# Performance work log

Measured on AMD Instinct MI355X. Metric: run time of the kernel, lower is better.

The kernel has to match this reference:

```python
import jax, jax.numpy as jnp
import numpy as np

VOCAB, TAGS, EDIM, HDIM = 50000, 9, 256, 512
H = HDIM // 2  # per-direction LSTM hidden
B, S = 64, 512


def setup_inputs() -> dict:
    key = jax.random.key(0)
    ks = jax.random.split(key, 16)
    sc = 0.05
    inp = {
        'sentence_batch': jax.random.randint(ks[0], (B, S), 0, VOCAB),
        'tags_batch': jax.random.randint(ks[1], (B, S), 0, TAGS),
        'mask': jnp.ones((B, S), dtype=bool),
        'emb': jax.random.normal(ks[2], (VOCAB, EDIM), jnp.float32) * sc,
        'w_ih_f': jax.random.normal(ks[3], (4 * H, EDIM), jnp.float32) * sc,
        'w_hh_f': jax.random.normal(ks[4], (4 * H, H), jnp.float32) * sc,
        'b_ih_f': jnp.zeros((4 * H,), jnp.float32),
        'b_hh_f': jnp.zeros((4 * H,), jnp.float32),
        'w_ih_b': jax.random.normal(ks[5], (4 * H, EDIM), jnp.float32) * sc,
        'w_hh_b': jax.random.normal(ks[6], (4 * H, H), jnp.float32) * sc,
        'b_ih_b': jnp.zeros((4 * H,), jnp.float32),
        'b_hh_b': jnp.zeros((4 * H,), jnp.float32),
        'w_out': jax.random.normal(ks[7], (TAGS, HDIM), jnp.float32) * sc,
        'b_out': jnp.zeros((TAGS,), jnp.float32),
        'start_trans': jax.random.uniform(ks[8], (TAGS,), jnp.float32, -0.1, 0.1),
        'end_trans': jax.random.uniform(ks[9], (TAGS,), jnp.float32, -0.1, 0.1),
        'trans': jax.random.uniform(ks[10], (TAGS, TAGS), jnp.float32, -0.1, 0.1),
    }
    return inp


def _lstm_dir(x, w_ih, w_hh, b_ih, b_hh):
    # x: [B,S,E] -> [B,S,H], torch gate order (i,f,g,o)
    b, h = x.shape[0], w_hh.shape[1]
    xg = jnp.einsum('bse,ge->bsg', x, w_ih) + b_ih + b_hh  # precompute input gates

    def step(carry, xg_t):
        hprev, cprev = carry
        g = xg_t + hprev @ w_hh.T
        i, f, gg, o = jnp.split(g, 4, axis=-1)
        c = jax.nn.sigmoid(f) * cprev + jax.nn.sigmoid(i) * jnp.tanh(gg)
        hnew = jax.nn.sigmoid(o) * jnp.tanh(c)
        return (hnew, c), hnew

    init = (jnp.zeros((b, h), x.dtype), jnp.zeros((b, h), x.dtype))
    _, hs = jax.lax.scan(step, init, jnp.swapaxes(xg, 0, 1))
    return jnp.swapaxes(hs, 0, 1)


def _crf_nll(emissions, tags, mask, start_trans, end_trans, trans):
    # emissions [B,S,T], tags [B,S], mask [B,S] bool. torchcrf llh, reduction='mean'.
    b, s, t = emissions.shape
    mf = mask.astype(emissions.dtype)
    # numerator score
    em_sc = jnp.take_along_axis(emissions, tags[..., None], axis=-1)[..., 0]  # [B,S]
    tr_sc = trans[tags[:, :-1], tags[:, 1:]]  # [B,S-1]
    score = start_trans[tags[:, 0]] + em_sc[:, 0]
    score = score + jnp.sum((tr_sc + em_sc[:, 1:]) * mf[:, 1:], axis=-1)
    seq_ends = jnp.sum(mask.astype(jnp.int32), axis=1) - 1
    last_tags = jnp.take_along_axis(tags, seq_ends[:, None], axis=1)[:, 0]
    score = score + end_trans[last_tags]
    # partition via forward algorithm (scan over time)
    alpha0 = start_trans[None, :] + emissions[:, 0]  # [B,T]

    def step(alpha, inputs):
        em_t, m_t = inputs  # [B,T], [B]
        nxt = jax.nn.logsumexp(alpha[:, :, None] + trans[None] + em_t[:, None, :], axis=1)
        alpha = jnp.where(m_t[:, None], nxt, alpha)
        return alpha, None

    em_tm = jnp.swapaxes(emissions[:, 1:], 0, 1)  # [S-1,B,T]
    m_tm = jnp.swapaxes(mask[:, 1:], 0, 1)  # [S-1,B]
    alpha, _ = jax.lax.scan(step, alpha0, (em_tm, m_tm))
    logZ = jax.nn.logsumexp(alpha + end_trans[None, :], axis=-1)
    llh = score - logZ
    return -jnp.mean(llh)


def reference(sentence_batch, tags_batch, mask, emb,
              w_ih_f, w_hh_f, b_ih_f, b_hh_f,
              w_ih_b, w_hh_b, b_ih_b, b_hh_b,
              w_out, b_out, start_trans, end_trans, trans):
    x = emb[sentence_batch]  # [B,S,E]
    hf = _lstm_dir(x, w_ih_f, w_hh_f, b_ih_f, b_hh_f)
    hb = _lstm_dir(x[:, ::-1], w_ih_b, w_hh_b, b_ih_b, b_hh_b)[:, ::-1]
    feats = jnp.concatenate([hf, hb], axis=-1) @ w_out.T + b_out  # [B,S,TAGS]
    return _crf_nll(feats, tags_batch, mask, start_trans, end_trans, trans)
```

## Files before the change

kernel.cpp:

```cpp
#include <hip/hip_runtime.h>
#include <stdint.h>

typedef unsigned short u16;
typedef __attribute__((ext_vector_type(4))) float f32x4;
typedef __attribute__((ext_vector_type(8))) short short8;
typedef __attribute__((ext_vector_type(8))) int v8i;

#define OFF_BIAS   ((size_t)0)
#define OFF_WFRAG  ((size_t)8192)
#define OFF_HHIST  ((size_t)1048576)
#define OFF_FEATS  ((size_t)34603008)
#define OFF_XG     ((size_t)37748736)

__device__ __forceinline__ u16 f2bf(float f) {
  union { float f; uint32_t u; } v; v.f = f;
  uint32_t u = v.u;
  return (u16)((u + 0x7fffu + ((u >> 16) & 1u)) >> 16);
}
__device__ __forceinline__ float bf2f(u16 h) {
  union { uint32_t u; float f; } v; v.u = ((uint32_t)h) << 16; return v.f;
}
__device__ __forceinline__ float bfh(uint32_t wrd, int hh) {
  return bf2f((u16)(wrd >> (16 * hh)));
}
__device__ __forceinline__ short8 pack8(f32x4 a, f32x4 b) {
  short8 r;
  r[0] = (short)f2bf(a[0]); r[1] = (short)f2bf(a[1]);
  r[2] = (short)f2bf(a[2]); r[3] = (short)f2bf(a[3]);
  r[4] = (short)f2bf(b[0]); r[5] = (short)f2bf(b[1]);
  r[6] = (short)f2bf(b[2]); r[7] = (short)f2bf(b[3]);
  return r;
}

__global__ void bias_kernel(const float* __restrict__ bihf, const float* __restrict__ bhhf,
                            const float* __restrict__ bihb, const float* __restrict__ bhhb,
                            float* __restrict__ bias) {
  int n = blockIdx.x * 256 + threadIdx.x;
  if (n < 1024) bias[n] = bihf[n] + bhhf[n];
  else          bias[n] = bihb[n - 1024] + bhhb[n - 1024];
}

__global__ void wfrag_prep_kernel(const float* __restrict__ whhf,
                                  const float* __restrict__ whhb,
                                  uint8_t* __restrict__ wfrag) {
  int gid = blockIdx.x * 256 + threadIdx.x;
  const int l    = gid & 63;
  const int kt   = (gid >> 6) & 7;
  const int gate = (gid >> 9) & 3;
  const int ubi  = (gid >> 11) & 1;
  const int w    = (gid >> 12) & 7;
  const int d    = (gid >> 15) & 1;
  const float* W = d ? whhb : whhf;
  const int n = l & 15, q = l >> 4;
  const int row = gate * 256 + w * 32 + ubi * 16 + n;
  uint32_t out[2] = {0u, 0u};
  #pragma unroll
  for (int jj = 0; jj < 4; ++jj) {
    const int k0 = kt * 32 + q * 8 + jj * 2;
    const int k1 = k0 + 1;
    const int u0 = (k0 >> 5) * 32 + (k0 & 1) * 16 + ((k0 & 31) >> 1);
    const int u1 = (k1 >> 5) * 32 + (k1 & 1) * 16 + ((k1 & 31) >> 1);
    const float f0 = W[(size_t)row * 256 + u0] * 16.0f;
    const float f1 = W[(size_t)row * 256 + u1] * 16.0f;
    const int pk = __builtin_amdgcn_cvt_pk_fp8_f32(f0, f1, 0, false);
    out[jj >> 1] |= (uint32_t)(pk & 0xffff) << (16 * (jj & 1));
  }
  const int p = kt >> 2, cc = kt & 3;
  const size_t addr =
      ((((size_t)((d * 8 + w) * 2 + ubi) * 4 + gate) * 2 + p) * 64 + l) * 32 + (size_t)cc * 8;
  *(uint2*)(wfrag + addr) = make_uint2(out[0], out[1]);
}

__global__ void __launch_bounds__(256) xg_gemm_kernel(
    const int* __restrict__ sent, const float* __restrict__ emb,
    const float* __restrict__ w_ih_f, const float* __restrict__ w_ih_b,
    const float* __restrict__ bias, u16* __restrict__ xgf)
{
  extern __shared__ char smem[];
  u16*   Al    = (u16*)smem;
  u16*   Bl    = (u16*)(smem + 34816);
  float* biasl = (float*)(smem + 69632);
  int*   tokl  = (int*)(smem + 70144);

  const int tid = threadIdx.x;
  const int d  = blockIdx.x >> 3, u0 = (blockIdx.x & 7) * 32;
  const int g  = blockIdx.y >> 6, qb = (blockIdx.y >> 4) & 3, s0 = (blockIdx.y & 15) * 32;
  const float* wih = d ? w_ih_b : w_ih_f;

  if (tid < 128) {
    tokl[tid]  = sent[(size_t)(g * 16 + qb * 4 + (tid & 3)) * 512 + s0 + (tid >> 2)];
    biasl[tid] = bias[d * 1024 + (tid >> 5) * 256 + u0 + (tid & 31)];
  }
  __syncthreads();

  f32x4 acc[4][4];
  #pragma unroll
  for (int i = 0; i < 4; ++i)
    #pragma unroll
    for (int j = 0; j < 4; ++j) acc[i][j] = (f32x4){0.f, 0.f, 0.f, 0.f};

  const int wv = tid >> 6, l = tid & 63;
  const int mh = (wv >> 1) * 64, nh = (wv & 1) * 64;
  const int fr = l & 15, fq = l >> 4;
  const int rr = tid >> 1, c0 = (tid & 1) * 64;

  for (int kc = 0; kc < 2; ++kc) {
    const int k0 = kc * 128;
    const float* asrc = emb + (size_t)tokl[rr] * 256 + k0 + c0;
    const float* bsrc = wih + (size_t)((rr >> 5) * 256 + u0 + (rr & 31)) * 256 + k0 + c0;
    u16* adst = Al + rr * 136 + c0;
    u16* bdst = Bl + rr * 136 + c0;
    #pragma unroll
    for (int gdx = 0; gdx < 8; ++gdx) {
      f32x4 a0 = *(const f32x4*)(asrc + gdx * 8);
      f32x4 a1 = *(const f32x4*)(asrc + gdx * 8 + 4);
      *(short8*)(adst + gdx * 8) = pack8(a0, a1);
      f32x4 b0 = *(const f32x4*)(bsrc + gdx * 8);
      f32x4 b1 = *(const f32x4*)(bsrc + gdx * 8 + 4);
      *(short8*)(bdst + gdx * 8) = pack8(b0, b1);
    }
    __syncthreads();
    #pragma unroll
    for (int ks = 0; ks < 4; ++ks) {
      short8 af[4], bfr[4];
      #pragma unroll
      for (int i = 0; i < 4; ++i)
        af[i] = *(const short8*)(Al + (mh + i * 16 + fr) * 136 + ks * 32 + fq * 8);
      #pragma unroll
      for (int j = 0; j < 4; ++j)
        bfr[j] = *(const short8*)(Bl + (nh + j * 16 + fr) * 136 + ks * 32 + fq * 8);
      #pragma unroll
      for (int i = 0; i < 4; ++i)
        #pragma unroll
        for (int j = 0; j < 4; ++j)
          acc[i][j] = __builtin_amdgcn_mfma_f32_16x16x32_bf16(af[i], bfr[j], acc[i][j], 0, 0, 0);
    }
    __syncthreads();
  }

  const float LOG2E = 1.4426950408889634f;
  const int g0 = nh >> 5;
  const float sA = (g0 == 2) ? (2.0f * LOG2E) : (-LOG2E);
  const int mh4 = mh >> 2;
  const int tid2 = (u0 >> 5) * 64 + qb * 16 + fr;
  u16* xbase = xgf + ((size_t)(d * 4 + g) * 512) * 16384;
  #pragma unroll
  for (int i = 0; i < 4; ++i) {
    const int s = s0 + mh4 + i * 4 + fq;
    #pragma unroll
    for (int nsub = 0; nsub < 2; ++nsub) {
      const int j0 = nsub, j1 = nsub + 2;
      const int cA = nh + j0 * 16 + fr, cB = nh + j1 * 16 + fr;
      short8 sv;
      #pragma unroll
      for (int r = 0; r < 4; ++r) {
        float vA = (acc[i][j0][r] + biasl[cA]) * sA;
        float vB = (acc[i][j1][r] + biasl[cB]) * (-LOG2E);
        sv[r]     = (short)f2bf(vA);
        sv[4 + r] = (short)f2bf(vB);
      }
      *(short8*)(xbase + (size_t)s * 16384 + tid2 * 32 + nsub * 16 + g0 * 4) = sv;
    }
  }
}

template<int CB, int PW>
__device__ __forceinline__ void lstm_step(
    int T, int d, int l, int q, int n, int w, int tid,
    const v8i (&wv)[2][4][2], float (&cst)[2][4],
    uint4& X0, uint4& X1, uint4& X2, uint4& X3,
    uint8_t* hx, const u16* xsl, u16* hhb)
{
  const int t_eff = d ? (511 - T) : T;

  int tn = T + 2; if (tn > 511) tn = 511;
  const int sn = d ? (511 - tn) : tn;
  const uint4* pf = (const uint4*)(xsl + (size_t)sn * 16384);
  const uint4 P0 = pf[0], P1 = pf[1], P2 = pf[2], P3 = pf[3];

  const uint8_t* hr = hx + CB * 4224 + (l & 15) * 264 + q * 8;
  const int2 b0 = *(const int2*)(hr +   0);
  const int2 b1 = *(const int2*)(hr +  32);
  const int2 b2 = *(const int2*)(hr +  64);
  const int2 b3 = *(const int2*)(hr +  96);
  const int2 b4 = *(const int2*)(hr + 128);
  const int2 b5 = *(const int2*)(hr + 160);
  const int2 b6 = *(const int2*)(hr + 192);
  const int2 b7 = *(const int2*)(hr + 224);
  const v8i A0 = (v8i){b0.x, b0.y, b1.x, b1.y, b2.x, b2.y, b3.x, b3.y};
  const v8i A1 = (v8i){b4.x, b4.y, b5.x, b5.y, b6.x, b6.y, b7.x, b7.y};

  f32x4 acc[2][4];
  #pragma unroll
  for (int ubi = 0; ubi < 2; ++ubi)
    #pragma unroll
    for (int gate = 0; gate < 4; ++gate) {
      f32x4 a = (f32x4){0.f, 0.f, 0.f, 0.f};
      a = __builtin_amdgcn_mfma_scale_f32_16x16x128_f8f6f4(
              A0, wv[ubi][gate][0], a, 0, 0, 0, 0x7f7f7f7f, 0, 0x7f7f7f7f);
      a = __builtin_amdgcn_mfma_scale_f32_16x16x128_f8f6f4(
              A1, wv[ubi][gate][1], a, 0, 0, 0, 0x7f7f7f7f, 0, 0x7f7f7f7f);
      acc[ubi][gate] = a;
    }

  const float Sm = -0.0056355275f;
  const float Sg =  0.0112710550f;
  const float K2 =  2.8853900818f;
  float hval[2][4];
  #pragma unroll
  for (int ubi = 0; ubi < 2; ++ubi) {
    const uint4& Xa = ubi ? X2 : X0;
    const uint4& Xb = ubi ? X3 : X1;
    #pragma unroll
    for (int r = 0; r < 4; ++r) {
      const uint32_t wi = (r < 2) ? Xa.x : Xa.y;
      const uint32_t wf = (r < 2) ? Xa.z : Xa.w;
      const uint32_t wg = (r < 2) ? Xb.x : Xb.y;
      const uint32_t wo = (r < 2) ? Xb.z : Xb.w;
      const int hp = r & 1;
      const float argi = fmaf(acc[ubi][0][r], Sm, bfh(wi, hp));
      const float argf = fmaf(acc[ubi][1][r], Sm, bfh(wf, hp));
      const float argg = fmaf(acc[ubi][2][r], Sg, bfh(wg, hp));
      const float argo = fmaf(acc[ubi][3][r], Sm, bfh(wo, hp));
      const float Ei = __builtin_amdgcn_exp2f(argi);
      const float Ef = __builtin_amdgcn_exp2f(argf);
      const float Eg = __builtin_amdgcn_exp2f(argg);
      const float Eo = __builtin_amdgcn_exp2f(argo);
      const float pf_ = 1.0f + Ef, pi_ = 1.0f + Ei, pg_ = 1.0f + Eg;
      const float P  = pi_ * pg_;
      const float rD = __builtin_amdgcn_rcpf(P * pf_);
      const float num = fmaf(cst[ubi][r], P, fmaf(Eg, pf_, -pf_));
      const float c   = num * rD;
      cst[ubi][r] = c;
      const float E2 = __builtin_amdgcn_exp2f(c * K2);
      const float rQ = __builtin_amdgcn_rcpf((1.0f + E2) * (1.0f + Eo));
      hval[ubi][r] = fmaf(E2, rQ, -rQ);
    }
  }

  {
    uint8_t* hw = hx + PW * 4224 + w * 32 + 2 * n;
    #pragma unroll
    for (int r = 0; r < 4; ++r) {
      const int pk = __builtin_amdgcn_cvt_pk_fp8_f32(hval[0][r] * 16.0f,
                                                     hval[1][r] * 16.0f, 0, false);
      *(u16*)(hw + (q * 4 + r) * 264) = (u16)(pk & 0xffff);
    }
  }

  asm volatile("s_waitcnt lgkmcnt(0)" ::: "memory");
  __builtin_amdgcn_s_barrier();
  __builtin_amdgcn_sched_barrier(0);

  {
    u16* hhs = hhb + (size_t)t_eff * 256;
    #pragma unroll
    for (int r = 0; r < 4; ++r) {
      uint32_t pb;
      asm("v_cvt_pk_bf16_f32 %0, %1, %2" : "=v"(pb) : "v"(hval[0][r]), "v"(hval[1][r]));
      hhs[(size_t)(q * 4 + r) * 512 * 256]      = (u16)(pb & 0xffffu);
      hhs[(size_t)(q * 4 + r) * 512 * 256 + 16] = (u16)(pb >> 16);
    }
  }

  X0 = P0; X1 = P1; X2 = P2; X3 = P3;
}

__global__ void __launch_bounds__(512, 2) lstm_kernel(
    const u16* __restrict__ xgf, const uint8_t* __restrict__ wfrag,
    u16* __restrict__ hhist)
{
  __shared__ uint8_t hx[2 * 16 * 264];

  const int tid = threadIdx.x;
  const int bid = blockIdx.x;
  const int d = bid >> 2, g = bid & 3;
  const int w = tid >> 6, l = tid & 63;
  const int n = l & 15, q = l >> 4;

  v8i wv[2][4][2];
  {
    const uint8_t* wb = wfrag + (size_t)(d * 8 + w) * 32768;
    #pragma unroll
    for (int ubi = 0; ubi < 2; ++ubi)
      #pragma unroll
      for (int gate = 0; gate < 4; ++gate)
        #pragma unroll
        for (int p = 0; p < 2; ++p) {
          const uint8_t* src = wb + ((size_t)(((ubi * 4 + gate) * 2 + p) * 64 + l)) * 32;
          const uint4 lo = *(const uint4*)(src);
          const uint4 hi = *(const uint4*)(src + 16);
          wv[ubi][gate][p] = (v8i){(int)lo.x, (int)lo.y, (int)lo.z, (int)lo.w,
                                   (int)hi.x, (int)hi.y, (int)hi.z, (int)hi.w};
        }
  }

  for (int i = tid; i < 2112; i += 512) ((uint32_t*)hx)[i] = 0u;

  const u16* xsl = xgf + (size_t)(d * 4 + g) * 512 * 16384 + (size_t)tid * 32;
  float cst[2][4] = {};
  u16* hhb = hhist + ((size_t)(d * 64 + g * 16) * 512) * 256 + (w * 32 + n);

  uint4 X0, X1, X2, X3, Y0, Y1, Y2, Y3;
  {
    const uint4* p0 = (const uint4*)(xsl + (size_t)(d ? 511 : 0) * 16384);
    X0 = p0[0]; X1 = p0[1]; X2 = p0[2]; X3 = p0[3];
    const uint4* p1 = (const uint4*)(xsl + (size_t)(d ? 510 : 1) * 16384);
    Y0 = p1[0]; Y1 = p1[1]; Y2 = p1[2]; Y3 = p1[3];
  }
  __syncthreads();

  for (int tt = 0; tt < 512; tt += 2) {
    lstm_step<0, 1>(tt,     d, l, q, n, w, tid, wv, cst, X0, X1, X2, X3, hx, xsl, hhb);
    lstm_step<1, 0>(tt + 1, d, l, q, n, w, tid, wv, cst, Y0, Y1, Y2, Y3, hx, xsl, hhb);
  }
}

__global__ void __launch_bounds__(256) proj_kernel(
    const u16* __restrict__ hhist, const float* __restrict__ w_out,
    const float* __restrict__ b_out, float* __restrict__ feats)
{
  __shared__ float wsm[9 * 512];
  __shared__ float bsm[9];
  const int tid = threadIdx.x;
  for (int i = tid; i < 4608; i += 256) wsm[i] = w_out[i];
  if (tid < 9) bsm[tid] = b_out[tid];
  __syncthreads();

  const int wv = tid >> 6, l = tid & 63;
  const int gw = blockIdx.x * 4 + wv;
  const int jb = l * 8;
  const int dd = jb >> 8;
  const int jloc = jb & 255;

  for (int qq = 0; qq < 8; ++qq) {
    const int pos = gw * 8 + qq;
    const int b = pos >> 9, s = pos & 511;
    const u16* hp = hhist + ((size_t)(dd * 64 + b) * 512 + s) * 256 + jloc;
    short8 hv8 = *(const short8*)hp;
    float hf[8];
    #pragma unroll
    for (int j = 0; j < 8; ++j) hf[j] = bf2f((u16)hv8[j]);
    float pt[9];
    #pragma unroll
    for (int tg2 = 0; tg2 < 9; ++tg2) {
      const float* wr = wsm + tg2 * 512 + jb;
      float a = 0.f;
      #pragma unroll
      for (int j = 0; j < 8; ++j) a = fmaf(hf[j], wr[j], a);
      pt[tg2] = a;
    }
    #pragma unroll
    for (int tg2 = 0; tg2 < 9; ++tg2)
      #pragma unroll
      for (int off = 32; off; off >>= 1)
        pt[tg2] += __shfl_xor(pt[tg2], off, 64);
    if (l == 0) {
      float* fo = feats + (size_t)pos * 9;
      #pragma unroll
      for (int tg2 = 0; tg2 < 9; ++tg2) fo[tg2] = pt[tg2] + bsm[tg2];
    }
  }
}

__global__ void __launch_bounds__(64) crf_kernel(
    const float* __restrict__ feats, const int* __restrict__ tags,
    const float* __restrict__ strans, const float* __restrict__ etrans,
    const float* __restrict__ trans, float* out)
{
  __shared__ float em[512 * 9];
  __shared__ float tr[81];
  __shared__ int   tg[512];
  const int b = blockIdx.x, l = threadIdx.x;
  const float* fb = feats + (size_t)b * 512 * 9;
  for (int i = l; i < 4608; i += 64) em[i] = fb[i];
  for (int i = l; i < 512; i += 64) tg[i] = tags[b * 512 + i];
  if (l < 81) tr[l] = trans[l];
  __syncthreads();

  float sc = 0.f;
  for (int s = 1 + l; s < 512; s += 64)
    sc += tr[tg[s - 1] * 9 + tg[s]] + em[s * 9 + tg[s]];
  #pragma unroll
  for (int off = 32; off; off >>= 1) sc += __shfl_xor(sc, off, 64);
  const float score = sc + strans[tg[0]] + em[tg[0]] + etrans[tg[511]];

  const int jj = (l < 9) ? l : 0;
  float al = (l < 9) ? (strans[l] + em[l]) : -1e30f;
  for (int t = 1; t < 512; ++t) {
    float ai[9];
    #pragma unroll
    for (int i = 0; i < 9; ++i) ai[i] = __shfl(al, i, 64);
    float m = ai[0];
    #pragma unroll
    for (int i = 1; i < 9; ++i) m = fmaxf(m, ai[i]);
    float ssum = 0.f;
    #pragma unroll
    for (int i = 0; i < 9; ++i) ssum += __expf(ai[i] + tr[i * 9 + jj] - m);
    al = em[t * 9 + jj] + m + __logf(ssum);
  }
  float v = (l < 9) ? (al + etrans[l]) : -3.0e38f;
  float m2 = v;
  #pragma unroll
  for (int off = 32; off; off >>= 1) m2 = fmaxf(m2, __shfl_xor(m2, off, 64));
  float ex = (l < 9) ? __expf(v - m2) : 0.f;
  #pragma unroll
  for (int off = 32; off; off >>= 1) ex += __shfl_xor(ex, off, 64);
  const float logZ = m2 + __logf(ex);
  if (l == 0) atomicAdd(out, -(score - logZ) * (1.0f / 64.0f));
}

extern "C" void kernel_launch(void* const* d_in, const int* in_sizes, int n_in,
                              void* d_out, int out_size, void* d_ws, size_t ws_size,
                              hipStream_t stream) {
  (void)in_sizes; (void)n_in; (void)out_size; (void)ws_size;
  const int*   sent = (const int*)d_in[0];
  const int*   tags = (const int*)d_in[1];
  const float* emb  = (const float*)d_in[3];
  const float* wihf = (const float*)d_in[4];
  const float* whhf = (const float*)d_in[5];
  const float* bihf = (const float*)d_in[6];
  const float* bhhf = (const float*)d_in[7];
  const float* wihb = (const float*)d_in[8];
  const float* whhb = (const float*)d_in[9];
  const float* bihb = (const float*)d_in[10];
  const float* bhhb = (const float*)d_in[11];
  const float* wout = (const float*)d_in[12];
  const float* bout = (const float*)d_in[13];
  const float* strn = (const float*)d_in[14];
  const float* etrn = (const float*)d_in[15];
  const float* trn  = (const float*)d_in[16];

  char* ws = (char*)d_ws;
  float*   biasb = (float*)(ws + OFF_BIAS);
  uint8_t* wfrag = (uint8_t*)(ws + OFF_WFRAG);
  u16*     hhist = (u16*)(ws + OFF_HHIST);
  float*   feats = (float*)(ws + OFF_FEATS);
  u16*     xgf   = (u16*)(ws + OFF_XG);
  float*   out   = (float*)d_out;

  hipMemsetAsync(d_out, 0, sizeof(float), stream);

  hipFuncSetAttribute(reinterpret_cast<const void*>(xg_gemm_kernel),
                      hipFuncAttributeMaxDynamicSharedMemorySize, 70656);

  bias_kernel<<<8, 256, 0, stream>>>(bihf, bhhf, bihb, bhhb, biasb);
  wfrag_prep_kernel<<<128, 256, 0, stream>>>(whhf, whhb, wfrag);
  xg_gemm_kernel<<<dim3(16, 256), 256, 70656, stream>>>(sent, emb, wihf, wihb, biasb, xgf);
  lstm_kernel<<<8, 512, 0, stream>>>(xgf, wfrag, hhist);
  proj_kernel<<<1024, 256, 0, stream>>>(hhist, wout, bout, feats);
  crf_kernel<<<64, 64, 0, stream>>>(feats, tags, strn, etrn, trn, out);
}
```

Baseline: 1.176 ms.

## Split LSTM recurrence across 16 waves per block and repack h layout

The recurrent LSTM kernel now launches 1024 threads per block instead of 512. Each wave handles one half (ubi) of a unit block, so per-step MFMA and gate math per wave is halved. The fp8 hidden-state exchange buffer is re-laid out to 272-byte rows so the A operand loads as two 16-byte reads instead of eight 8-byte reads, and the xg prefetch distance drops from two steps to one. Bf16 packing in the xg GEMM epilogue now uses the hardware packed convert instead of software rounding. The cost is more waves joining each per-step barrier, byte-granular LDS stores, and less prefetch slack to hide global latency on a serial critical path.

```diff
diff --git a/kernel.cpp b/kernel.cpp
--- a/kernel.cpp
+++ b/kernel.cpp
@@ -23,13 +23,18 @@
 __device__ __forceinline__ float bfh(uint32_t wrd, int hh) {
   return bf2f((u16)(wrd >> (16 * hh)));
 }
+__device__ __forceinline__ uint32_t cvtpk_bf16(float lo, float hi) {
+  uint32_t r;
+  asm("v_cvt_pk_bf16_f32 %0, %1, %2" : "=v"(r) : "v"(lo), "v"(hi));
+  return r;
+}
 __device__ __forceinline__ short8 pack8(f32x4 a, f32x4 b) {
-  short8 r;
-  r[0] = (short)f2bf(a[0]); r[1] = (short)f2bf(a[1]);
-  r[2] = (short)f2bf(a[2]); r[3] = (short)f2bf(a[3]);
-  r[4] = (short)f2bf(b[0]); r[5] = (short)f2bf(b[1]);
-  r[6] = (short)f2bf(b[2]); r[7] = (short)f2bf(b[3]);
-  return r;
+  union { short8 s; uint32_t u[4]; } r;
+  r.u[0] = cvtpk_bf16(a[0], a[1]);
+  r.u[1] = cvtpk_bf16(a[2], a[3]);
+  r.u[2] = cvtpk_bf16(b[0], b[1]);
+  r.u[3] = cvtpk_bf16(b[2], b[3]);
+  return r.s;
 }
 
 __global__ void bias_kernel(const float* __restrict__ bihf, const float* __restrict__ bhhf,
@@ -151,101 +156,98 @@
     for (int nsub = 0; nsub < 2; ++nsub) {
       const int j0 = nsub, j1 = nsub + 2;
       const int cA = nh + j0 * 16 + fr, cB = nh + j1 * 16 + fr;
-      short8 sv;
+      float vA[4], vB[4];
       #pragma unroll
       for (int r = 0; r < 4; ++r) {
-        float vA = (acc[i][j0][r] + biasl[cA]) * sA;
-        float vB = (acc[i][j1][r] + biasl[cB]) * (-LOG2E);
-        sv[r]     = (short)f2bf(vA);
-        sv[4 + r] = (short)f2bf(vB);
+        vA[r] = (acc[i][j0][r] + biasl[cA]) * sA;
+        vB[r] = (acc[i][j1][r] + biasl[cB]) * (-LOG2E);
       }
-      *(short8*)(xbase + (size_t)s * 16384 + tid2 * 32 + nsub * 16 + g0 * 4) = sv;
+      union { short8 s8; uint32_t u[4]; } sv;
+      sv.u[0] = cvtpk_bf16(vA[0], vA[1]);
+      sv.u[1] = cvtpk_bf16(vA[2], vA[3]);
+      sv.u[2] = cvtpk_bf16(vB[0], vB[1]);
+      sv.u[3] = cvtpk_bf16(vB[2], vB[3]);
+      *(short8*)(xbase + (size_t)s * 16384 + tid2 * 32 + nsub * 16 + g0 * 4) = sv.s8;
     }
   }
 }
 
 template<int CB, int PW>
 __device__ __forceinline__ void lstm_step(
-    int T, int d, int l, int q, int n, int w, int tid,
-    const v8i (&wv)[2][4][2], float (&cst)[2][4],
-    uint4& X0, uint4& X1, uint4& X2, uint4& X3,
-    uint8_t* hx, const u16* xsl, u16* hhb)
+    int T, int d, int l, int q, int n,
+    const v8i (&wvr)[4][2], float (&cst)[4],
+    uint4& X0, uint4& X1,
+    uint8_t* hx, const u16* xsl, u16* hhb, int pub_off)
 {
   const int t_eff = d ? (511 - T) : T;
 
-  int tn = T + 2; if (tn > 511) tn = 511;
+  int tn = T + 1; if (tn > 511) tn = 511;
   const int sn = d ? (511 - tn) : tn;
-  const uint4* pf = (const uint4*)(xsl + (size_t)sn * 16384);
-  const uint4 P0 = pf[0], P1 = pf[1], P2 = pf[2], P3 = pf[3];
-
-  const uint8_t* hr = hx + CB * 4224 + (l & 15) * 264 + q * 8;
-  const int2 b0 = *(const int2*)(hr +   0);
-  const int2 b1 = *(const int2*)(hr +  32);
-  const int2 b2 = *(const int2*)(hr +  64);
-  const int2 b3 = *(const int2*)(hr +  96);
-  const int2 b4 = *(const int2*)(hr + 128);
-  const int2 b5 = *(const int2*)(hr + 160);
-  const int2 b6 = *(const int2*)(hr + 192);
-  const int2 b7 = *(const int2*)(hr + 224);
-  const v8i A0 = (v8i){b0.x, b0.y, b1.x, b1.y, b2.x, b2.y, b3.x, b3.y};
-  const v8i A1 = (v8i){b4.x, b4.y, b5.x, b5.y, b6.x, b6.y, b7.x, b7.y};
-
-  f32x4 acc[2][4];
-  #pragma unroll
-  for (int ubi = 0; ubi < 2; ++ubi)
-    #pragma unroll
-    for (int gate = 0; gate < 4; ++gate) {
-      f32x4 a = (f32x4){0.f, 0.f, 0.f, 0.f};
-      a = __builtin_amdgcn_mfma_scale_f32_16x16x128_f8f6f4(
-              A0, wv[ubi][gate][0], a, 0, 0, 0, 0x7f7f7f7f, 0, 0x7f7f7f7f);
-      a = __builtin_amdgcn_mfma_scale_f32_16x16x128_f8f6f4(
-              A1, wv[ubi][gate][1], a, 0, 0, 0, 0x7f7f7f7f, 0, 0x7f7f7f7f);
-      acc[ubi][gate] = a;
-    }
+  const uint4* pfp = (const uint4*)(xsl + (size_t)sn * 16384);
+  const uint4 P0 = pfp[0], P1 = pfp[1];
+
+  const uint8_t* hr = hx + CB * 4352 + (l & 15) * 272 + q * 32;
+  f32x4 acc[4];
+  {
+    const uint4 alo = *(const uint4*)(hr);
+    const uint4 ahi = *(const uint4*)(hr + 16);
+    const v8i A0 = (v8i){(int)alo.x, (int)alo.y, (int)alo.z, (int)alo.w,
+                         (int)ahi.x, (int)ahi.y, (int)ahi.z, (int)ahi.w};
+    #pragma unroll
+    for (int gate = 0; gate < 4; ++gate)
+      acc[gate] = __builtin_amdgcn_mfma_scale_f32_16x16x128_f8f6f4(
+          A0, wvr[gate][0], (f32x4){0.f, 0.f, 0.f, 0.f},
+          0, 0, 0, 0x7f7f7f7f, 0, 0x7f7f7f7f);
+  }
+  {
+    const uint4 alo = *(const uint4*)(hr + 128);
+    const uint4 ahi = *(const uint4*)(hr + 144);
+    const v8i A1 = (v8i){(int)alo.x, (int)alo.y, (int)alo.z, (int)alo.w,
+                         (int)ahi.x, (int)ahi.y, (int)ahi.z, (int)ahi.w};
+    #pragma unroll
+    for (int gate = 0; gate < 4; ++gate)
+      acc[gate] = __builtin_amdgcn_mfma_scale_f32_16x16x128_f8f6f4(
+          A1, wvr[gate][1], acc[gate], 0, 0, 0, 0x7f7f7f7f, 0, 0x7f7f7f7f);
+  }
 
   const float Sm = -0.0056355275f;
   const float Sg =  0.0112710550f;
   const float K2 =  2.8853900818f;
-  float hval[2][4];
-  #pragma unroll
-  for (int ubi = 0; ubi < 2; ++ubi) {
-    const uint4& Xa = ubi ? X2 : X0;
-    const uint4& Xb = ubi ? X3 : X1;
-    #pragma unroll
-    for (int r = 0; r < 4; ++r) {
-      const uint32_t wi = (r < 2) ? Xa.x : Xa.y;
-      const uint32_t wf = (r < 2) ? Xa.z : Xa.w;
-      const uint32_t wg = (r < 2) ? Xb.x : Xb.y;
-      const uint32_t wo = (r < 2) ? Xb.z : Xb.w;
-      const int hp = r & 1;
-      const float argi = fmaf(acc[ubi][0][r], Sm, bfh(wi, hp));
-      const float argf = fmaf(acc[ubi][1][r], Sm, bfh(wf, hp));
-      const float argg = fmaf(acc[ubi][2][r], Sg, bfh(wg, hp));
-      const float argo = fmaf(acc[ubi][3][r], Sm, bfh(wo, hp));
-      const float Ei = __builtin_amdgcn_exp2f(argi);
-      const float Ef = __builtin_amdgcn_exp2f(argf);
-      const float Eg = __builtin_amdgcn_exp2f(argg);
-      const float Eo = __builtin_amdgcn_exp2f(argo);
-      const float pf_ = 1.0f + Ef, pi_ = 1.0f + Ei, pg_ = 1.0f + Eg;
-      const float P  = pi_ * pg_;
-      const float rD = __builtin_amdgcn_rcpf(P * pf_);
-      const float num = fmaf(cst[ubi][r], P, fmaf(Eg, pf_, -pf_));
-      const float c   = num * rD;
-      cst[ubi][r] = c;
-      const float E2 = __builtin_amdgcn_exp2f(c * K2);
-      const float rQ = __builtin_amdgcn_rcpf((1.0f + E2) * (1.0f + Eo));
-      hval[ubi][r] = fmaf(E2, rQ, -rQ);
-    }
-  }
-
-  {
-    uint8_t* hw = hx + PW * 4224 + w * 32 + 2 * n;
-    #pragma unroll
-    for (int r = 0; r < 4; ++r) {
-      const int pk = __builtin_amdgcn_cvt_pk_fp8_f32(hval[0][r] * 16.0f,
-                                                     hval[1][r] * 16.0f, 0, false);
-      *(u16*)(hw + (q * 4 + r) * 264) = (u16)(pk & 0xffff);
-    }
+  float hval[4];
+  #pragma unroll
+  for (int r = 0; r < 4; ++r) {
+    const uint32_t wi = (r < 2) ? X0.x : X0.y;
+    const uint32_t wf = (r < 2) ? X0.z : X0.w;
+    const uint32_t wg = (r < 2) ? X1.x : X1.y;
+    const uint32_t wo = (r < 2) ? X1.z : X1.w;
+    const int hp = r & 1;
+    const float argi = fmaf(acc[0][r], Sm, bfh(wi, hp));
+    const float argf = fmaf(acc[1][r], Sm, bfh(wf, hp));
+    const float argg = fmaf(acc[2][r], Sg, bfh(wg, hp));
+    const float argo = fmaf(acc[3][r], Sm, bfh(wo, hp));
+    const float Ei = __builtin_amdgcn_exp2f(argi);
+    const float Ef = __builtin_amdgcn_exp2f(argf);
+    const float Eg = __builtin_amdgcn_exp2f(argg);
+    const float Eo = __builtin_amdgcn_exp2f(argo);
+    const float pf_ = 1.0f + Ef, pi_ = 1.0f + Ei, pg_ = 1.0f + Eg;
+    const float P  = pi_ * pg_;
+    const float rD = __builtin_amdgcn_rcpf(P * pf_);
+    const float num = fmaf(cst[r], P, fmaf(Eg, pf_, -pf_));
+    const float c   = num * rD;
+    cst[r] = c;
+    const float E2 = __builtin_amdgcn_exp2f(c * K2);
+    const float rQ = __builtin_amdgcn_rcpf((1.0f + E2) * (1.0f + Eo));
+    hval[r] = fmaf(E2, rQ, -rQ);
+  }
+
+  {
+    uint8_t* hw = hx + PW * 4352 + pub_off;
+    const int pk01 = __builtin_amdgcn_cvt_pk_fp8_f32(hval[0] * 16.0f, hval[1] * 16.0f, 0, false);
+    const int pk23 = __builtin_amdgcn_cvt_pk_fp8_f32(hval[2] * 16.0f, hval[3] * 16.0f, 0, false);
+    hw[(q * 4 + 0) * 272] = (uint8_t)(pk01 & 0xff);
+    hw[(q * 4 + 1) * 272] = (uint8_t)((pk01 >> 8) & 0xff);
+    hw[(q * 4 + 2) * 272] = (uint8_t)(pk23 & 0xff);
+    hw[(q * 4 + 3) * 272] = (uint8_t)((pk23 >> 8) & 0xff);
   }
 
   asm volatile("s_waitcnt lgkmcnt(0)" ::: "memory");
@@ -254,65 +256,65 @@
 
   {
     u16* hhs = hhb + (size_t)t_eff * 256;
-    #pragma unroll
-    for (int r = 0; r < 4; ++r) {
-      uint32_t pb;
-      asm("v_cvt_pk_bf16_f32 %0, %1, %2" : "=v"(pb) : "v"(hval[0][r]), "v"(hval[1][r]));
-      hhs[(size_t)(q * 4 + r) * 512 * 256]      = (u16)(pb & 0xffffu);
-      hhs[(size_t)(q * 4 + r) * 512 * 256 + 16] = (u16)(pb >> 16);
-    }
-  }
-
-  X0 = P0; X1 = P1; X2 = P2; X3 = P3;
-}
-
-__global__ void __launch_bounds__(512, 2) lstm_kernel(
+    const uint32_t pb01 = cvtpk_bf16(hval[0], hval[1]);
+    const uint32_t pb23 = cvtpk_bf16(hval[2], hval[3]);
+    hhs[(size_t)(q * 4 + 0) * 131072] = (u16)(pb01 & 0xffffu);
+    hhs[(size_t)(q * 4 + 1) * 131072] = (u16)(pb01 >> 16);
+    hhs[(size_t)(q * 4 + 2) * 131072] = (u16)(pb23 & 0xffffu);
+    hhs[(size_t)(q * 4 + 3) * 131072] = (u16)(pb23 >> 16);
+  }
+
+  X0 = P0; X1 = P1;
+}
+
+__global__ void __launch_bounds__(1024, 4) lstm_kernel(
     const u16* __restrict__ xgf, const uint8_t* __restrict__ wfrag,
     u16* __restrict__ hhist)
 {
-  __shared__ uint8_t hx[2 * 16 * 264];
+  __shared__ uint8_t hx[2 * 16 * 272];
 
   const int tid = threadIdx.x;
   const int bid = blockIdx.x;
   const int d = bid >> 2, g = bid & 3;
-  const int w = tid >> 6, l = tid & 63;
+  const int w2 = tid >> 6, l = tid & 63;
   const int n = l & 15, q = l >> 4;
-
-  v8i wv[2][4][2];
-  {
-    const uint8_t* wb = wfrag + (size_t)(d * 8 + w) * 32768;
-    #pragma unroll
-    for (int ubi = 0; ubi < 2; ++ubi)
-      #pragma unroll
-      for (int gate = 0; gate < 4; ++gate)
-        #pragma unroll
-        for (int p = 0; p < 2; ++p) {
-          const uint8_t* src = wb + ((size_t)(((ubi * 4 + gate) * 2 + p) * 64 + l)) * 32;
-          const uint4 lo = *(const uint4*)(src);
-          const uint4 hi = *(const uint4*)(src + 16);
-          wv[ubi][gate][p] = (v8i){(int)lo.x, (int)lo.y, (int)lo.z, (int)lo.w,
-                                   (int)hi.x, (int)hi.y, (int)hi.z, (int)hi.w};
-        }
-  }
-
-  for (int i = tid; i < 2112; i += 512) ((uint32_t*)hx)[i] = 0u;
-
-  const u16* xsl = xgf + (size_t)(d * 4 + g) * 512 * 16384 + (size_t)tid * 32;
-  float cst[2][4] = {};
-  u16* hhb = hhist + ((size_t)(d * 64 + g * 16) * 512) * 256 + (w * 32 + n);
-
-  uint4 X0, X1, X2, X3, Y0, Y1, Y2, Y3;
+  const int wo = w2 >> 1, ubi = w2 & 1;
+
+  v8i wvr[4][2];
+  {
+    const uint8_t* wb = wfrag + (size_t)(d * 8 + wo) * 32768;
+    #pragma unroll
+    for (int gate = 0; gate < 4; ++gate)
+      #pragma unroll
+      for (int p = 0; p < 2; ++p) {
+        const uint8_t* src = wb + ((size_t)(((ubi * 4 + gate) * 2 + p) * 64 + l)) * 32;
+        const uint4 lo = *(const uint4*)(src);
+        const uint4 hi = *(const uint4*)(src + 16);
+        wvr[gate][p] = (v8i){(int)lo.x, (int)lo.y, (int)lo.z, (int)lo.w,
+                             (int)hi.x, (int)hi.y, (int)hi.z, (int)hi.w};
+      }
+  }
+
+  for (int i = tid; i < 2176; i += 1024) ((uint32_t*)hx)[i] = 0u;
+
+  const u16* xsl = xgf + (size_t)(d * 4 + g) * 512 * 16384
+                 + ((size_t)(wo * 64 + l)) * 32 + ubi * 16;
+  float cst[4] = {};
+  u16* hhb = hhist + ((size_t)(d * 64 + g * 16) * 512) * 256 + (w2 * 16 + n);
+
+  const int kk = wo * 32 + 2 * n + ubi;
+  const int pub_off = (kk >> 7) * 128 + ((kk >> 3) & 3) * 32 + ((kk >> 5) & 3) * 8 + (kk & 7);
+
+  uint4 X0, X1;
   {
     const uint4* p0 = (const uint4*)(xsl + (size_t)(d ? 511 : 0) * 16384);
-    X0 = p0[0]; X1 = p0[1]; X2 = p0[2]; X3 = p0[3];
-    const uint4* p1 = (const uint4*)(xsl + (size_t)(d ? 510 : 1) * 16384);
-    Y0 = p1[0]; Y1 = p1[1]; Y2 = p1[2]; Y3 = p1[3];
+    X0 = p0[0]; X1 = p0[1];
   }
   __syncthreads();
 
   for (int tt = 0; tt < 512; tt += 2) {
-    lstm_step<0, 1>(tt,     d, l, q, n, w, tid, wv, cst, X0, X1, X2, X3, hx, xsl, hhb);
-    lstm_step<1, 0>(tt + 1, d, l, q, n, w, tid, wv, cst, Y0, Y1, Y2, Y3, hx, xsl, hhb);
+    lstm_step<0, 1>(tt,     d, l, q, n, wvr, cst, X0, X1, hx, xsl, hhb, pub_off);
+    lstm_step<1, 0>(tt + 1, d, l, q, n, wvr, cst, X0, X1, hx, xsl, hhb, pub_off);
   }
 }
 
@@ -447,7 +449,7 @@
   bias_kernel<<<8, 256, 0, stream>>>(bihf, bhhf, bihb, bhhb, biasb);
   wfrag_prep_kernel<<<128, 256, 0, stream>>>(whhf, whhb, wfrag);
   xg_gemm_kernel<<<dim3(16, 256), 256, 70656, stream>>>(sent, emb, wihf, wihb, biasb, xgf);
-  lstm_kernel<<<8, 512, 0, stream>>>(xgf, wfrag, hhist);
+  lstm_kernel<<<8, 1024, 0, stream>>>(xgf, wfrag, hhist);
   proj_kernel<<<1024, 256, 0, stream>>>(hhist, wout, bout, feats);
   crf_kernel<<<64, 64, 0, stream>>>(feats, tags, strn, etrn, trn, out);
 }
```

New measurement: 2.076 ms. 1.77x slower.
